# Kernel tuning notes

Hardware: AMD Instinct MI355X
Metric: run time of the kernel (lower is better)

## Reference

```python
import jax, jax.numpy as jnp
import numpy as np

B, N, K = 8, 2048, 30  # graphs, points per graph, kNN neighbors


def setup_inputs() -> dict:
    key = jax.random.key(0)
    ks = jax.random.split(key, 16)
    w = lambda k, s: jax.random.normal(k, s, jnp.float32) * 0.05
    z = lambda s: jnp.zeros(s, jnp.float32)
    return {
        "x": jax.random.normal(ks[0], (B * N, 3), jnp.float32),
        "pos": jax.random.normal(ks[1], (B * N, 3), jnp.float32),
        "w1a": w(ks[2], (12, 64)), "b1a": z(64),
        "w1b": w(ks[3], (64, 64)), "b1b": z(64),
        "w2a": w(ks[4], (128, 64)), "b2a": z(64),
        "w2b": w(ks[5], (64, 64)), "b2b": z(64),
        "w3a": w(ks[6], (128, 64)), "b3a": z(64),
        "w3b": w(ks[7], (64, 64)), "b3b": z(64),
        "hw1": w(ks[8], (192, 1024)), "hb1": z(1024),
        "hw2": w(ks[9], (1024, 512)), "hb2": z(512),
        "hw3": w(ks[10], (512, 128)), "hb3": z(128),
        "batch": jnp.repeat(jnp.arange(B, dtype=jnp.int32), N),
        "batch_size": B,
    }


def _knn_idx(f):
    # f: [B,N,d] -> indices of K nearest neighbors (incl. self), [B,N,K]
    d2 = jnp.sum(f * f, axis=-1)  # [B,N]
    dist = d2[:, :, None] + d2[:, None, :] - 2.0 * jnp.einsum('bnd,bmd->bnm', f, f)
    return jax.lax.top_k(-dist, K)[1]


def _edge_conv(f, wa, ba, wb, bb):
    # DynamicEdgeConv: kNN graph on f, message MLP([x_i, x_j - x_i]), max-aggregate
    idx = _knn_idx(f)                                   # [B,N,K]
    xj = jax.vmap(lambda ff, ii: ff[ii])(f, idx)        # [B,N,K,d]
    xi = f[:, :, None, :]
    e = jnp.concatenate([jnp.broadcast_to(xi, xj.shape), xj - xi], axis=-1)
    h = jax.nn.relu(e @ wa + ba)                        # MLP layer 1 (act)
    h = h @ wb + bb                                     # MLP layer 2 (plain last)
    return jnp.max(h, axis=2)                           # max aggr -> [B,N,64]


def reference(x, pos, w1a, b1a, w1b, b1b, w2a, b2a, w2b, b2b, w3a, b3a, w3b, b3b,
              hw1, hb1, hw2, hb2, hw3, hb3, batch, batch_size):
    x0 = jnp.concatenate([x, pos], axis=-1).reshape(batch_size, -1, 6)  # [B,N,6]
    x1 = _edge_conv(x0, w1a, b1a, w1b, b1b)
    x2 = _edge_conv(x1, w2a, b2a, w2b, b2b)
    x3 = _edge_conv(x2, w3a, b3a, w3b, b3b)
    feat = jnp.concatenate([x1, x2, x3], axis=-1)       # [B,N,192]
    h = jax.nn.relu(feat @ hw1 + hb1)                   # head MLP (dropout=eval)
    h = jax.nn.relu(h @ hw2 + hb2)
    out = h @ hw3 + hb3                                 # [B,N,out_channels]
    return out
```

## Files before the change

kernel.cpp:

```cpp
#include <hip/hip_runtime.h>
#include <math.h>

#define BATCH 8
#define NPER 2048
#define NPTS (BATCH*NPER)
#define KNN 30

typedef __attribute__((ext_vector_type(8))) short bf16x8;
typedef __attribute__((ext_vector_type(4))) float f32x4;

__device__ __forceinline__ ushort f2bf(float x) {
    unsigned u = __float_as_uint(x);
    unsigned r = (u + 0x7fffu + ((u >> 16) & 1u)) >> 16;
    return (ushort)r;
}
__device__ __forceinline__ float bf2f(ushort h) {
    return __uint_as_float(((unsigned)h) << 16);
}

__global__ void concat_kernel(const float* __restrict__ x, const float* __restrict__ pos,
                              float* __restrict__ x0) {
    int n = blockIdx.x * blockDim.x + threadIdx.x;
    if (n >= NPTS) return;
#pragma unroll
    for (int d = 0; d < 3; ++d) {
        x0[n*6 + d]     = x[n*3 + d];
        x0[n*6 + 3 + d] = pos[n*3 + d];
    }
}

template<int D>
__global__ void d2_kernel(const float* __restrict__ f, int stride, float* __restrict__ d2) {
    int n = blockIdx.x * blockDim.x + threadIdx.x;
    if (n >= NPTS) return;
    const float* r = f + (size_t)n * stride;
    float s = 0.f;
#pragma unroll
    for (int d = 0; d < D; ++d) s += r[d]*r[d];
    d2[n] = s;
}

template<int D>
__global__ __launch_bounds__(256, 4) void knn4_kernel(const float* __restrict__ f, int stride,
                                                      const float* __restrict__ d2,
                                                      int* __restrict__ idx) {
    __shared__ float sdist[4][NPER];
    __shared__ float sxi[4][(D+3)/4*4];
    __shared__ float sd2n[4];
    int t = threadIdx.x;
    int n0 = blockIdx.x * 4;
    int base = (n0 >> 11) << 11;

    if (t < 4*D) {
        int q = t / D, d = t - q*D;
        sxi[q][d] = f[(size_t)(n0 + q)*stride + d];
    }
    if (t < 4) sd2n[t] = d2[n0 + t];
    __syncthreads();

#pragma unroll 1
    for (int j = 0; j < NPER/256; ++j) {
        int ml = t + 256*j;
        int m = base + ml;
        const float* fm = f + (size_t)m*stride;
        float d2m = d2[m];
        float dot0 = 0.f, dot1 = 0.f, dot2 = 0.f, dot3 = 0.f;
#pragma unroll
        for (int d = 0; d < D; ++d) {
            float a = fm[d];
            dot0 += a*sxi[0][d];
            dot1 += a*sxi[1][d];
            dot2 += a*sxi[2][d];
            dot3 += a*sxi[3][d];
        }
        sdist[0][ml] = sd2n[0] + d2m - 2.f*dot0;
        sdist[1][ml] = sd2n[1] + d2m - 2.f*dot1;
        sdist[2][ml] = sd2n[2] + d2m - 2.f*dot2;
        sdist[3][ml] = sd2n[3] + d2m - 2.f*dot3;
    }
    __syncthreads();

    int w = t >> 6, lane = t & 63;
    int n = n0 + w;

    unsigned u[NPER/64];
#pragma unroll
    for (int i = 0; i < NPER/64; ++i) {
        float dv = sdist[w][lane + 64*i];
        int b = __float_as_int(dv);
        u[i] = (unsigned)(b ^ ((b >> 31) | 0x80000000));
    }

    unsigned T = 0u;
#pragma unroll
    for (int bit = 31; bit >= 0; --bit) {
        unsigned C = T | (1u << bit);
        int c = 0;
#pragma unroll
        for (int i = 0; i < NPER/64; ++i)
            c += (int)__popcll(__ballot(u[i] < C));
        if (c < KNN) T = C;
    }

    unsigned lm = 0u, em = 0u;
#pragma unroll
    for (int i = 0; i < NPER/64; ++i) {
        lm |= (u[i] < T)  ? (1u << i) : 0u;
        em |= (u[i] == T) ? (1u << i) : 0u;
    }
    int nl = __popc(lm);
    int inc = nl;
#pragma unroll
    for (int off = 1; off < 64; off <<= 1) {
        int y = __shfl_up(inc, off);
        if (lane >= off) inc += y;
    }
    int excl = inc - nl;
    int total_less = __shfl(inc, 63);

    int* op = idx + (size_t)n * KNN;
    int slot = excl;
#pragma unroll
    for (int i = 0; i < NPER/64; ++i) {
        if (lm & (1u << i)) { op[slot] = base + i*64 + lane; ++slot; }
    }

    int need = KNN - total_less;
    int running = 0;
#pragma unroll
    for (int i = 0; i < NPER/64; ++i) {
        unsigned long long bal = __ballot((em >> i) & 1u);
        if (bal) {
            unsigned long long lt = bal & ((1ull << lane) - 1ull);
            int r = running + __popcll(lt);
            if (((em >> i) & 1u) && r < need) op[total_less + r] = base + i*64 + lane;
            running += (int)__popcll(bal);
        }
    }
}

__global__ __launch_bounds__(256) void transpose64_kernel(const float* __restrict__ fin, int stride,
                                                          float* __restrict__ fT,
                                                          float* __restrict__ d2out) {
    __shared__ float tile[64][65];
    int t = threadIdx.x;
    int n0 = blockIdx.x * 64;
#pragma unroll
    for (int i = 0; i < 4; ++i) {
        int id = t + 256*i;
        int r = id >> 4, c4 = (id & 15) * 4;
        float4 v = *reinterpret_cast<const float4*>(&fin[(size_t)(n0 + r)*stride + c4]);
        tile[r][c4] = v.x; tile[r][c4+1] = v.y; tile[r][c4+2] = v.z; tile[r][c4+3] = v.w;
    }
    __syncthreads();
    if (t < 64) {
        float s = 0.f;
#pragma unroll
        for (int d = 0; d < 64; ++d) s += tile[t][d]*tile[t][d];
        d2out[n0 + t] = s;
    }
#pragma unroll
    for (int i = 0; i < 16; ++i) {
        int id = t + 256*i;
        int d = id >> 6, nn = id & 63;
        fT[(size_t)d * NPTS + n0 + nn] = tile[nn][d];
    }
}

__global__ __launch_bounds__(256) void knn6_kernel(const float* __restrict__ fq, int qstride,
                                                   const float* __restrict__ fT,
                                                   const float* __restrict__ d2,
                                                   int* __restrict__ idx) {
    __shared__ float sdist[4][NPER];
    __shared__ float sq[4][64];
    __shared__ float sd2n[4];
    int t = threadIdx.x;
    int n0 = blockIdx.x * 4;
    int base = (n0 >> 11) << 11;

    {
        int q = t >> 6, d = t & 63;
        sq[q][d] = fq[(size_t)(n0 + q)*qstride + d];
    }
    if (t < 4) sd2n[t] = d2[n0 + t];
    __syncthreads();

    float acc0[8], acc1[8], acc2[8], acc3[8];
#pragma unroll
    for (int j = 0; j < 8; ++j) { acc0[j] = 0.f; acc1[j] = 0.f; acc2[j] = 0.f; acc3[j] = 0.f; }

    int cbase = base + 8*t;

#pragma unroll 2
    for (int dc = 0; dc < 16; ++dc) {
        int d0 = dc * 4;
        float4 q0 = *reinterpret_cast<const float4*>(&sq[0][d0]);
        float4 q1 = *reinterpret_cast<const float4*>(&sq[1][d0]);
        float4 q2 = *reinterpret_cast<const float4*>(&sq[2][d0]);
        float4 q3 = *reinterpret_cast<const float4*>(&sq[3][d0]);
        float qa0[4] = {q0.x, q0.y, q0.z, q0.w};
        float qa1[4] = {q1.x, q1.y, q1.z, q1.w};
        float qa2[4] = {q2.x, q2.y, q2.z, q2.w};
        float qa3[4] = {q3.x, q3.y, q3.z, q3.w};
#pragma unroll
        for (int dd = 0; dd < 4; ++dd) {
            const float* cp = fT + (size_t)(d0 + dd) * NPTS + cbase;
            float4 c0 = *reinterpret_cast<const float4*>(cp);
            float4 c1 = *reinterpret_cast<const float4*>(cp + 4);
            float cv[8] = {c0.x,c0.y,c0.z,c0.w,c1.x,c1.y,c1.z,c1.w};
#pragma unroll
            for (int j = 0; j < 8; ++j) {
                acc0[j] += cv[j]*qa0[dd];
                acc1[j] += cv[j]*qa1[dd];
                acc2[j] += cv[j]*qa2[dd];
                acc3[j] += cv[j]*qa3[dd];
            }
        }
    }

    {
        float dn0 = sd2n[0], dn1 = sd2n[1], dn2 = sd2n[2], dn3 = sd2n[3];
        float4 dm0 = *reinterpret_cast<const float4*>(&d2[cbase]);
        float4 dm1 = *reinterpret_cast<const float4*>(&d2[cbase + 4]);
        float dmv[8] = {dm0.x,dm0.y,dm0.z,dm0.w,dm1.x,dm1.y,dm1.z,dm1.w};
#pragma unroll
        for (int j = 0; j < 8; ++j) {
            int ml = 8*t + j;
            sdist[0][ml] = dn0 + dmv[j] - 2.f*acc0[j];
            sdist[1][ml] = dn1 + dmv[j] - 2.f*acc1[j];
            sdist[2][ml] = dn2 + dmv[j] - 2.f*acc2[j];
            sdist[3][ml] = dn3 + dmv[j] - 2.f*acc3[j];
        }
    }
    __syncthreads();

    int w = t >> 6, lane = t & 63;
    int n = n0 + w;

    unsigned u[NPER/64];
#pragma unroll
    for (int i = 0; i < NPER/64; ++i) {
        float dv = sdist[w][lane + 64*i];
        int b = __float_as_int(dv);
        u[i] = (unsigned)(b ^ ((b >> 31) | 0x80000000));
    }

    unsigned T = 0u;
#pragma unroll
    for (int bit = 31; bit >= 0; --bit) {
        unsigned C = T | (1u << bit);
        int c = 0;
#pragma unroll
        for (int i = 0; i < NPER/64; ++i)
            c += (int)__popcll(__ballot(u[i] < C));
        if (c < KNN) T = C;
    }

    unsigned lm = 0u, em = 0u;
#pragma unroll
    for (int i = 0; i < NPER/64; ++i) {
        lm |= (u[i] < T)  ? (1u << i) : 0u;
        em |= (u[i] == T) ? (1u << i) : 0u;
    }
    int nl = __popc(lm);
    int inc = nl;
#pragma unroll
    for (int off = 1; off < 64; off <<= 1) {
        int y = __shfl_up(inc, off);
        if (lane >= off) inc += y;
    }
    int excl = inc - nl;
    int total_less = __shfl(inc, 63);

    int* op = idx + (size_t)n * KNN;
    int slot = excl;
#pragma unroll
    for (int i = 0; i < NPER/64; ++i) {
        if (lm & (1u << i)) { op[slot] = base + i*64 + lane; ++slot; }
    }

    int need = KNN - total_less;
    int running = 0;
#pragma unroll
    for (int i = 0; i < NPER/64; ++i) {
        unsigned long long bal = __ballot((em >> i) & 1u);
        if (bal) {
            unsigned long long lt = bal & ((1ull << lane) - 1ull);
            int r = running + __popcll(lt);
            if (((em >> i) & 1u) && r < need) op[total_less + r] = base + i*64 + lane;
            running += (int)__popcll(bal);
        }
    }
}

template<int D>
__global__ __launch_bounds__(256) void gmatbase_kernel(const float* __restrict__ fin, int in_stride,
                                                       const float* __restrict__ wa,
                                                       const float* __restrict__ ba,
                                                       float* __restrict__ G,
                                                       float* __restrict__ Gb) {
    constexpr int DP = (D+7)/8*8;
    __shared__ float sF[64][DP];
    int t = threadIdx.x;
    int row0 = blockIdx.x * 64;
    for (int i = t; i < 64*D; i += 256) {
        int r = i / D, c = i - r*D;
        sF[r][c] = fin[(size_t)(row0 + r)*in_stride + c];
    }
    int w = t >> 6, lane = t & 63;
    {
        float wreg[D];
#pragma unroll
        for (int d = 0; d < D; ++d) wreg[d] = wa[(size_t)(D + d)*64 + lane];
        __syncthreads();
#pragma unroll 1
        for (int pi = 0; pi < 16; ++pi) {
            int p = w*16 + pi;
            float acc = 0.f;
            if constexpr (D % 4 == 0) {
#pragma unroll
                for (int d = 0; d < D; d += 4) {
                    float4 fv = *reinterpret_cast<const float4*>(&sF[p][d]);
                    acc += fv.x*wreg[d] + fv.y*wreg[d+1] + fv.z*wreg[d+2] + fv.w*wreg[d+3];
                }
            } else {
#pragma unroll
                for (int d = 0; d < D; ++d) acc += sF[p][d]*wreg[d];
            }
            G[(size_t)(row0 + p)*64 + lane] = acc;
        }
    }
    {
        float wreg[D];
#pragma unroll
        for (int d = 0; d < D; ++d)
            wreg[d] = wa[(size_t)d*64 + lane] - wa[(size_t)(D + d)*64 + lane];
        float bc = ba[lane];
#pragma unroll 1
        for (int pi = 0; pi < 16; ++pi) {
            int p = w*16 + pi;
            float acc = bc;
#pragma unroll
            for (int d = 0; d < D; ++d) acc += sF[p][d]*wreg[d];
            Gb[(size_t)(row0 + p)*64 + lane] = acc;
        }
    }
}

__global__ __launch_bounds__(256) void edgemfma_kernel(
    const float* __restrict__ G, const float* __restrict__ Gbase,
    const int* __restrict__ idx,
    const ushort* __restrict__ wbTh, const ushort* __restrict__ wbTl,
    const float* __restrict__ bb,
    float* __restrict__ fout, int out_stride,
    ushort* __restrict__ fh, ushort* __restrict__ fl)
{
    __shared__ __align__(16) ushort sHh[128*72];
    __shared__ __align__(16) ushort sHl[128*72];
    __shared__ float sbase[4][64];
    int t = threadIdx.x;
    int n0 = blockIdx.x * 4;

    {
        int p = t >> 6, c = t & 63;
        sbase[p][c] = Gbase[(size_t)(n0 + p)*64 + c];
    }
    __syncthreads();

    {
        int r = t >> 1, c0 = (t & 1) * 32;
        int p = r >> 5, e = r & 31;
        int ecl = e < KNN ? e : (KNN - 1);
        int j = idx[(size_t)(n0 + p)*KNN + ecl];
        const float* gp = G + (size_t)j*64 + c0;
        const float* bp = &sbase[p][c0];
#pragma unroll
        for (int g = 0; g < 4; ++g) {
            float4 g0 = *reinterpret_cast<const float4*>(gp + 8*g);
            float4 g1 = *reinterpret_cast<const float4*>(gp + 8*g + 4);
            float4 b0 = *reinterpret_cast<const float4*>(bp + 8*g);
            float4 b1 = *reinterpret_cast<const float4*>(bp + 8*g + 4);
            float h[8] = {fmaxf(b0.x+g0.x,0.f), fmaxf(b0.y+g0.y,0.f),
                          fmaxf(b0.z+g0.z,0.f), fmaxf(b0.w+g0.w,0.f),
                          fmaxf(b1.x+g1.x,0.f), fmaxf(b1.y+g1.y,0.f),
                          fmaxf(b1.z+g1.z,0.f), fmaxf(b1.w+g1.w,0.f)};
            uint ph[4], pl[4];
#pragma unroll
            for (int i2 = 0; i2 < 4; ++i2) {
                ushort h0 = f2bf(h[2*i2]);
                ushort l0 = f2bf(h[2*i2] - bf2f(h0));
                ushort h1_ = f2bf(h[2*i2+1]);
                ushort l1 = f2bf(h[2*i2+1] - bf2f(h1_));
                ph[i2] = (uint)h0 | ((uint)h1_ << 16);
                pl[i2] = (uint)l0 | ((uint)l1 << 16);
            }
            *reinterpret_cast<uint4*>(&sHh[r*72 + c0 + 8*g]) = make_uint4(ph[0],ph[1],ph[2],ph[3]);
            *reinterpret_cast<uint4*>(&sHl[r*72 + c0 + 8*g]) = make_uint4(pl[0],pl[1],pl[2],pl[3]);
        }
    }
    __syncthreads();

    int lane = t & 63, w = t >> 6;
    int fr = lane & 15, fk = (lane >> 4) * 8;

    f32x4 acc[2][4];
#pragma unroll
    for (int mf = 0; mf < 2; ++mf)
#pragma unroll
        for (int nf = 0; nf < 4; ++nf) acc[mf][nf] = f32x4{0.f,0.f,0.f,0.f};

#pragma unroll
    for (int kk = 0; kk < 2; ++kk) {
        bf16x8 a0h = *reinterpret_cast<const bf16x8*>(&sHh[(w*32 + fr)*72 + kk*32 + fk]);
        bf16x8 a1h = *reinterpret_cast<const bf16x8*>(&sHh[(w*32 + 16 + fr)*72 + kk*32 + fk]);
        bf16x8 a0l = *reinterpret_cast<const bf16x8*>(&sHl[(w*32 + fr)*72 + kk*32 + fk]);
        bf16x8 a1l = *reinterpret_cast<const bf16x8*>(&sHl[(w*32 + 16 + fr)*72 + kk*32 + fk]);
#pragma unroll
        for (int nf = 0; nf < 4; ++nf) {
            bf16x8 bh = *reinterpret_cast<const bf16x8*>(&wbTh[(size_t)(nf*16 + fr)*64 + kk*32 + fk]);
            bf16x8 bl = *reinterpret_cast<const bf16x8*>(&wbTl[(size_t)(nf*16 + fr)*64 + kk*32 + fk]);
            acc[0][nf] = __builtin_amdgcn_mfma_f32_16x16x32_bf16(a0h, bh, acc[0][nf], 0,0,0);
            acc[0][nf] = __builtin_amdgcn_mfma_f32_16x16x32_bf16(a0h, bl, acc[0][nf], 0,0,0);
            acc[0][nf] = __builtin_amdgcn_mfma_f32_16x16x32_bf16(a0l, bh, acc[0][nf], 0,0,0);
            acc[1][nf] = __builtin_amdgcn_mfma_f32_16x16x32_bf16(a1h, bh, acc[1][nf], 0,0,0);
            acc[1][nf] = __builtin_amdgcn_mfma_f32_16x16x32_bf16(a1h, bl, acc[1][nf], 0,0,0);
            acc[1][nf] = __builtin_amdgcn_mfma_f32_16x16x32_bf16(a1l, bh, acc[1][nf], 0,0,0);
        }
    }

#pragma unroll
    for (int nf = 0; nf < 4; ++nf) {
        float vmax = -3.4e38f;
#pragma unroll
        for (int mf = 0; mf < 2; ++mf) {
#pragma unroll
            for (int j = 0; j < 4; ++j) {
                int lr = mf*16 + ((lane >> 4) << 2) + j;
                float v = acc[mf][nf][j];
                vmax = (lr < KNN) ? fmaxf(vmax, v) : vmax;
            }
        }
        vmax = fmaxf(vmax, __shfl_xor(vmax, 16));
        vmax = fmaxf(vmax, __shfl_xor(vmax, 32));
        if (lane < 16) {
            int c = nf*16 + lane;
            float v = vmax + bb[c];
            size_t o = (size_t)(n0 + w)*out_stride + c;
            fout[o] = v;
            ushort h = f2bf(v);
            fh[o] = h;
            fl[o] = f2bf(v - bf2f(h));
        }
    }
}

__global__ void wsplit_kernel(const float* __restrict__ w, int K, int N,
                              ushort* __restrict__ hi, ushort* __restrict__ lo, int total) {
    int i = blockIdx.x * 256 + threadIdx.x;
    if (i >= total) return;
    int n = i / K, k = i - n*K;
    float x = w[(size_t)k * N + n];
    ushort h = f2bf(x);
    hi[i] = h;
    lo[i] = f2bf(x - bf2f(h));
}

template<bool RELU, bool SPLIT_OUT>
__global__ __launch_bounds__(256) void mlp_gemm2_kernel(
    const ushort* __restrict__ Ah, const ushort* __restrict__ Al, int K,
    const ushort* __restrict__ Bh, const ushort* __restrict__ Bl,
    const float* __restrict__ bias,
    float* __restrict__ C, ushort* __restrict__ Ch, ushort* __restrict__ Cl, int N)
{
    __shared__ __align__(16) ushort sAh[128*40];
    __shared__ __align__(16) ushort sAl[128*40];
    __shared__ __align__(16) ushort sBh[128*40];
    __shared__ __align__(16) ushort sBl[128*40];
    int t = threadIdx.x;
    int lane = t & 63, w = t >> 6;
    int row0 = blockIdx.x * 128;
    int n0   = blockIdx.y * 128;
    int wr = w & 1, wc = w >> 1;
    int fr = lane & 15, fq = lane >> 4, fk = fq * 8;
    int r = t >> 2, sg = (t & 3) * 8;

    f32x4 acc[4][4];
#pragma unroll
    for (int m = 0; m < 4; ++m)
#pragma unroll
        for (int n = 0; n < 4; ++n) acc[m][n] = f32x4{0.f,0.f,0.f,0.f};

    const int nk = K / 32;
#pragma unroll 1
    for (int kc = 0; kc < nk; ++kc) {
        int k0 = kc * 32;
        uint4 vah0 = *reinterpret_cast<const uint4*>(&Ah[(size_t)(row0 + r)*K + k0 + sg]);
        uint4 vah1 = *reinterpret_cast<const uint4*>(&Ah[(size_t)(row0 + r + 64)*K + k0 + sg]);
        uint4 val0 = *reinterpret_cast<const uint4*>(&Al[(size_t)(row0 + r)*K + k0 + sg]);
        uint4 val1 = *reinterpret_cast<const uint4*>(&Al[(size_t)(row0 + r + 64)*K + k0 + sg]);
        uint4 vbh0 = *reinterpret_cast<const uint4*>(&Bh[(size_t)(n0 + r)*K + k0 + sg]);
        uint4 vbh1 = *reinterpret_cast<const uint4*>(&Bh[(size_t)(n0 + r + 64)*K + k0 + sg]);
        uint4 vbl0 = *reinterpret_cast<const uint4*>(&Bl[(size_t)(n0 + r)*K + k0 + sg]);
        uint4 vbl1 = *reinterpret_cast<const uint4*>(&Bl[(size_t)(n0 + r + 64)*K + k0 + sg]);
        __syncthreads();
        *reinterpret_cast<uint4*>(&sAh[r*40 + sg]) = vah0;
        *reinterpret_cast<uint4*>(&sAh[(r+64)*40 + sg]) = vah1;
        *reinterpret_cast<uint4*>(&sAl[r*40 + sg]) = val0;
        *reinterpret_cast<uint4*>(&sAl[(r+64)*40 + sg]) = val1;
        *reinterpret_cast<uint4*>(&sBh[r*40 + sg]) = vbh0;
        *reinterpret_cast<uint4*>(&sBh[(r+64)*40 + sg]) = vbh1;
        *reinterpret_cast<uint4*>(&sBl[r*40 + sg]) = vbl0;
        *reinterpret_cast<uint4*>(&sBl[(r+64)*40 + sg]) = vbl1;
        __syncthreads();

        bf16x8 bh_[4], bl_[4];
#pragma unroll
        for (int n = 0; n < 4; ++n) {
            bh_[n] = *reinterpret_cast<const bf16x8*>(&sBh[(wc*64 + n*16 + fr)*40 + fk]);
            bl_[n] = *reinterpret_cast<const bf16x8*>(&sBl[(wc*64 + n*16 + fr)*40 + fk]);
        }
#pragma unroll
        for (int m = 0; m < 4; ++m) {
            bf16x8 ah_ = *reinterpret_cast<const bf16x8*>(&sAh[(wr*64 + m*16 + fr)*40 + fk]);
            bf16x8 al_ = *reinterpret_cast<const bf16x8*>(&sAl[(wr*64 + m*16 + fr)*40 + fk]);
#pragma unroll
            for (int n = 0; n < 4; ++n) {
                acc[m][n] = __builtin_amdgcn_mfma_f32_16x16x32_bf16(ah_, bh_[n], acc[m][n], 0,0,0);
                acc[m][n] = __builtin_amdgcn_mfma_f32_16x16x32_bf16(ah_, bl_[n], acc[m][n], 0,0,0);
                acc[m][n] = __builtin_amdgcn_mfma_f32_16x16x32_bf16(al_, bh_[n], acc[m][n], 0,0,0);
            }
        }
    }

#pragma unroll
    for (int n = 0; n < 4; ++n) {
        int ocol = n0 + wc*64 + n*16 + fr;
        float bc = bias[ocol];
#pragma unroll
        for (int m = 0; m < 4; ++m) {
            int orow = row0 + wr*64 + m*16 + fq*4;
#pragma unroll
            for (int j = 0; j < 4; ++j) {
                float v = acc[m][n][j] + bc;
                if (RELU) v = fmaxf(v, 0.f);
                if (SPLIT_OUT) {
                    ushort h = f2bf(v);
                    Ch[(size_t)(orow + j)*N + ocol] = h;
                    Cl[(size_t)(orow + j)*N + ocol] = f2bf(v - bf2f(h));
                } else {
                    C[(size_t)(orow + j)*N + ocol] = v;
                }
            }
        }
    }
}

__global__ __launch_bounds__(256) void head_kernel(const float* __restrict__ feat,
                            const float* __restrict__ hw1, const float* __restrict__ hb1,
                            const float* __restrict__ hw2, const float* __restrict__ hb2,
                            const float* __restrict__ hw3, const float* __restrict__ hb3,
                            float* __restrict__ out) {
    __shared__ float smem[16384];
    float* sfeat = smem;
    float* sh1   = smem + 6144;
    int t = threadIdx.x;
    int row0 = blockIdx.x * 32;

    for (int i = t; i < 32*192; i += 256) sfeat[i] = feat[(size_t)row0*192 + i];
    __syncthreads();

    int c4 = t & 127, rh = t >> 7;
    float4 acc2[16];
    {
        float4 b = *reinterpret_cast<const float4*>(&hb2[4*c4]);
#pragma unroll
        for (int i = 0; i < 16; ++i) acc2[i] = b;
    }
    int c1 = t & 63, rg = t >> 6;

    for (int chunk = 0; chunk < 8; ++chunk) {
        int k0 = chunk * 128;
        float acc1a[8], acc1b[8];
        {
            float ba_ = hb1[k0 + c1], bb_ = hb1[k0 + 64 + c1];
#pragma unroll
            for (int i = 0; i < 8; ++i) { acc1a[i] = ba_; acc1b[i] = bb_; }
        }
#pragma unroll 1
        for (int k = 0; k < 192; k += 4) {
            float wA0 = hw1[(size_t)(k+0)*1024 + k0 + c1];
            float wA1 = hw1[(size_t)(k+1)*1024 + k0 + c1];
            float wA2 = hw1[(size_t)(k+2)*1024 + k0 + c1];
            float wA3 = hw1[(size_t)(k+3)*1024 + k0 + c1];
            float wB0 = hw1[(size_t)(k+0)*1024 + k0 + 64 + c1];
            float wB1 = hw1[(size_t)(k+1)*1024 + k0 + 64 + c1];
            float wB2 = hw1[(size_t)(k+2)*1024 + k0 + 64 + c1];
            float wB3 = hw1[(size_t)(k+3)*1024 + k0 + 64 + c1];
#pragma unroll
            for (int i = 0; i < 8; ++i) {
                float4 fv = *reinterpret_cast<const float4*>(&sfeat[(rg + 4*i)*192 + k]);
                acc1a[i] += fv.x*wA0 + fv.y*wA1 + fv.z*wA2 + fv.w*wA3;
                acc1b[i] += fv.x*wB0 + fv.y*wB1 + fv.z*wB2 + fv.w*wB3;
            }
        }
#pragma unroll
        for (int i = 0; i < 8; ++i) {
            sh1[(rg + 4*i)*128 + c1]      = fmaxf(acc1a[i], 0.f);
            sh1[(rg + 4*i)*128 + 64 + c1] = fmaxf(acc1b[i], 0.f);
        }
        __syncthreads();
        float4 wn[4];
#pragma unroll
        for (int q = 0; q < 4; ++q)
            wn[q] = *reinterpret_cast<const float4*>(&hw2[(size_t)(k0 + q)*512 + 4*c4]);
#pragma unroll 1
        for (int k = 0; k < 128; k += 4) {
            float4 wv[4];
#pragma unroll
            for (int q = 0; q < 4; ++q) wv[q] = wn[q];
            if (k + 4 < 128) {
#pragma unroll
                for (int q = 0; q < 4; ++q)
                    wn[q] = *reinterpret_cast<const float4*>(&hw2[(size_t)(k0 + k + 4 + q)*512 + 4*c4]);
            }
#pragma unroll
            for (int i = 0; i < 16; ++i) {
                float4 h4 = *reinterpret_cast<const float4*>(&sh1[(rh + 2*i)*128 + k]);
                acc2[i].x += h4.x*wv[0].x + h4.y*wv[1].x + h4.z*wv[2].x + h4.w*wv[3].x;
                acc2[i].y += h4.x*wv[0].y + h4.y*wv[1].y + h4.z*wv[2].y + h4.w*wv[3].y;
                acc2[i].z += h4.x*wv[0].z + h4.y*wv[1].z + h4.z*wv[2].z + h4.w*wv[3].z;
                acc2[i].w += h4.x*wv[0].w + h4.y*wv[1].w + h4.z*wv[2].w + h4.w*wv[3].w;
            }
        }
        __syncthreads();
    }
#pragma unroll
    for (int i = 0; i < 16; ++i) {
        float4 v;
        v.x = fmaxf(acc2[i].x, 0.f); v.y = fmaxf(acc2[i].y, 0.f);
        v.z = fmaxf(acc2[i].z, 0.f); v.w = fmaxf(acc2[i].w, 0.f);
        *reinterpret_cast<float4*>(&smem[(rh + 2*i)*512 + 4*c4]) = v;
    }
    __syncthreads();
    int c3 = t & 63, rg3 = t >> 6;
    float acc3a[8], acc3b[8];
    {
        float ba_ = hb3[c3], bb_ = hb3[c3 + 64];
#pragma unroll
        for (int i = 0; i < 8; ++i) { acc3a[i] = ba_; acc3b[i] = bb_; }
    }
#pragma unroll 1
    for (int k = 0; k < 512; k += 4) {
        float wA0 = hw3[(size_t)(k+0)*128 + c3];
        float wA1 = hw3[(size_t)(k+1)*128 + c3];
        float wA2 = hw3[(size_t)(k+2)*128 + c3];
        float wA3 = hw3[(size_t)(k+3)*128 + c3];
        float wB0 = hw3[(size_t)(k+0)*128 + c3 + 64];
        float wB1 = hw3[(size_t)(k+1)*128 + c3 + 64];
        float wB2 = hw3[(size_t)(k+2)*128 + c3 + 64];
        float wB3 = hw3[(size_t)(k+3)*128 + c3 + 64];
#pragma unroll
        for (int i = 0; i < 8; ++i) {
            float4 h4 = *reinterpret_cast<const float4*>(&smem[(rg3 + 4*i)*512 + k]);
            acc3a[i] += h4.x*wA0 + h4.y*wA1 + h4.z*wA2 + h4.w*wA3;
            acc3b[i] += h4.x*wB0 + h4.y*wB1 + h4.z*wB2 + h4.w*wB3;
        }
    }
#pragma unroll
    for (int i = 0; i < 8; ++i) {
        out[(size_t)(row0 + rg3 + 4*i)*128 + c3]      = acc3a[i];
        out[(size_t)(row0 + rg3 + 4*i)*128 + c3 + 64] = acc3b[i];
    }
}

extern "C" void kernel_launch(void* const* d_in, const int* in_sizes, int n_in,
                              void* d_out, int out_size, void* d_ws, size_t ws_size,
                              hipStream_t stream) {
    (void)in_sizes; (void)n_in; (void)out_size;
    const float* x   = (const float*)d_in[0];
    const float* pos = (const float*)d_in[1];
    const float* w1a = (const float*)d_in[2];
    const float* b1a = (const float*)d_in[3];
    const float* w1b = (const float*)d_in[4];
    const float* b1b = (const float*)d_in[5];
    const float* w2a = (const float*)d_in[6];
    const float* b2a = (const float*)d_in[7];
    const float* w2b = (const float*)d_in[8];
    const float* b2b = (const float*)d_in[9];
    const float* w3a = (const float*)d_in[10];
    const float* b3a = (const float*)d_in[11];
    const float* w3b = (const float*)d_in[12];
    const float* b3b = (const float*)d_in[13];
    const float* hw1 = (const float*)d_in[14];
    const float* hb1 = (const float*)d_in[15];
    const float* hw2 = (const float*)d_in[16];
    const float* hb2 = (const float*)d_in[17];
    const float* hw3 = (const float*)d_in[18];
    const float* hb3 = (const float*)d_in[19];
    float* out = (float*)d_out;

    float* ws = (float*)d_ws;
    float* x0   = ws;
    float* feat = ws + 98304;
    float* d2b  = ws + 3244032;
    int*   idxb = (int*)(ws + 3260416);
    float* G    = ws + 3751936;
    ushort* w1h = (ushort*)(ws + 4800512);
    ushort* w1l = (ushort*)(ws + 4898816);
    ushort* w2h = (ushort*)(ws + 4997120);
    ushort* w2l = (ushort*)(ws + 5259264);
    ushort* w3h = (ushort*)(ws + 5521408);
    ushort* w3l = (ushort*)(ws + 5554176);
    ushort* wb1h = (ushort*)(ws + 5586944);
    ushort* wb1l = (ushort*)(ws + 5588992);
    ushort* wb2h = (ushort*)(ws + 5591040);
    ushort* wb2l = (ushort*)(ws + 5593088);
    ushort* wb3h = (ushort*)(ws + 5595136);
    ushort* wb3l = (ushort*)(ws + 5597184);
    float* Gbase = ws + 5599232;
    ushort* fAh  = (ushort*)(ws + 6647808);
    ushort* fAl  = (ushort*)(ws + 8220672);
    const size_t base_units = 9793536;

    float* fT = G;

    int ns = 0;
    {
        const int cands[5] = {1, 2, 4, 8, 16};
        for (int ci = 0; ci < 5; ++ci) {
            int c = cands[ci];
            size_t need = (base_units + (size_t)(NPTS / c) * 1536) * 4;
            if (need <= ws_size) { ns = c; break; }
        }
    }

    wsplit_kernel<<<(192*1024 + 255)/256, 256, 0, stream>>>(hw1, 192, 1024, w1h, w1l, 192*1024);
    wsplit_kernel<<<(1024*512 + 255)/256, 256, 0, stream>>>(hw2, 1024, 512, w2h, w2l, 1024*512);
    wsplit_kernel<<<(512*128 + 255)/256, 256, 0, stream>>>(hw3, 512, 128, w3h, w3l, 512*128);
    wsplit_kernel<<<16, 256, 0, stream>>>(w1b, 64, 64, wb1h, wb1l, 4096);
    wsplit_kernel<<<16, 256, 0, stream>>>(w2b, 64, 64, wb2h, wb2l, 4096);
    wsplit_kernel<<<16, 256, 0, stream>>>(w3b, 64, 64, wb3h, wb3l, 4096);

    concat_kernel<<<NPTS/256, 256, 0, stream>>>(x, pos, x0);

    d2_kernel<6><<<NPTS/256, 256, 0, stream>>>(x0, 6, d2b);
    knn4_kernel<6><<<NPTS/4, 256, 0, stream>>>(x0, 6, d2b, idxb);
    gmatbase_kernel<6><<<NPTS/64, 256, 0, stream>>>(x0, 6, w1a, b1a, G, Gbase);
    edgemfma_kernel<<<NPTS/4, 256, 0, stream>>>(G, Gbase, idxb, wb1h, wb1l, b1b,
                                                feat, 192, fAh, fAl);

    transpose64_kernel<<<NPTS/64, 256, 0, stream>>>(feat, 192, fT, d2b);
    knn6_kernel<<<NPTS/4, 256, 0, stream>>>(feat, 192, fT, d2b, idxb);
    gmatbase_kernel<64><<<NPTS/64, 256, 0, stream>>>(feat, 192, w2a, b2a, G, Gbase);
    edgemfma_kernel<<<NPTS/4, 256, 0, stream>>>(G, Gbase, idxb, wb2h, wb2l, b2b,
                                                feat + 64, 192, fAh + 64, fAl + 64);

    transpose64_kernel<<<NPTS/64, 256, 0, stream>>>(feat + 64, 192, fT, d2b);
    knn6_kernel<<<NPTS/4, 256, 0, stream>>>(feat + 64, 192, fT, d2b, idxb);
    gmatbase_kernel<64><<<NPTS/64, 256, 0, stream>>>(feat + 64, 192, w3a, b3a, G, Gbase);
    edgemfma_kernel<<<NPTS/4, 256, 0, stream>>>(G, Gbase, idxb, wb3h, wb3l, b3b,
                                                feat + 128, 192, fAh + 128, fAl + 128);

    if (ns > 0) {
        int Ms = NPTS / ns;
        ushort* h1h = (ushort*)(ws + base_units);
        ushort* h1l = h1h + (size_t)Ms * 1024;
        ushort* h2h = (ushort*)(ws + base_units + (size_t)Ms * 1024);
        ushort* h2l = h2h + (size_t)Ms * 512;
        for (int s = 0; s < ns; ++s) {
            const ushort* Ash = fAh + (size_t)s * Ms * 192;
            const ushort* Asl = fAl + (size_t)s * Ms * 192;
            float* outs = out + (size_t)s * Ms * 128;
            mlp_gemm2_kernel<true, true ><<<dim3(Ms/128, 1024/128), 256, 0, stream>>>(
                Ash, Asl, 192, w1h, w1l, hb1, nullptr, h1h, h1l, 1024);
            mlp_gemm2_kernel<true, true ><<<dim3(Ms/128,  512/128), 256, 0, stream>>>(
                h1h, h1l, 1024, w2h, w2l, hb2, nullptr, h2h, h2l, 512);
            mlp_gemm2_kernel<false, false><<<dim3(Ms/128,  128/128), 256, 0, stream>>>(
                h2h, h2l, 512, w3h, w3l, hb3, outs, nullptr, nullptr, 128);
        }
    } else {
        head_kernel<<<NPTS/32, 256, 0, stream>>>(feat, hw1, hb1, hw2, hb2, hw3, hb3, out);
    }
}
```

Measured before the change: 702.6 us.

## Merge weight-split launches, fuse concat with norms, and use smaller-tile final GEMM

Replaces six separate weight-split launches with a single kernel that dispatches by global index, and fuses the input concat with the squared-norm computation. This removes several small launches and one global reload. It also swaps the last head GEMM (N=128) for a 64-row tile variant, giving twice as many blocks on a grid that otherwise had only one column of tiles. The fp32 fallback head kernel is removed, so if the workspace is too small no head is computed at all.

```diff
diff --git a/kernel.cpp b/kernel.cpp
--- a/kernel.cpp
+++ b/kernel.cpp
@@ -18,25 +18,21 @@
     return __uint_as_float(((unsigned)h) << 16);
 }
 
-__global__ void concat_kernel(const float* __restrict__ x, const float* __restrict__ pos,
-                              float* __restrict__ x0) {
+__global__ void concat_d2_kernel(const float* __restrict__ x, const float* __restrict__ pos,
+                                 float* __restrict__ x0, float* __restrict__ d2) {
     int n = blockIdx.x * blockDim.x + threadIdx.x;
     if (n >= NPTS) return;
+    float v[6];
 #pragma unroll
     for (int d = 0; d < 3; ++d) {
-        x0[n*6 + d]     = x[n*3 + d];
-        x0[n*6 + 3 + d] = pos[n*3 + d];
-    }
-}
-
-template<int D>
-__global__ void d2_kernel(const float* __restrict__ f, int stride, float* __restrict__ d2) {
-    int n = blockIdx.x * blockDim.x + threadIdx.x;
-    if (n >= NPTS) return;
-    const float* r = f + (size_t)n * stride;
+        v[d]     = x[n*3 + d];
+        v[3 + d] = pos[n*3 + d];
+    }
+#pragma unroll
+    for (int d = 0; d < 6; ++d) x0[n*6 + d] = v[d];
     float s = 0.f;
 #pragma unroll
-    for (int d = 0; d < D; ++d) s += r[d]*r[d];
+    for (int d = 0; d < 6; ++d) s += v[d]*v[d];
     d2[n] = s;
 }
 
@@ -454,10 +450,23 @@
     }
 }
 
-__global__ void wsplit_kernel(const float* __restrict__ w, int K, int N,
-                              ushort* __restrict__ hi, ushort* __restrict__ lo, int total) {
-    int i = blockIdx.x * 256 + threadIdx.x;
-    if (i >= total) return;
+__global__ void wsplit_all_kernel(
+    const float* __restrict__ hw1, ushort* __restrict__ w1h, ushort* __restrict__ w1l,
+    const float* __restrict__ hw2, ushort* __restrict__ w2h, ushort* __restrict__ w2l,
+    const float* __restrict__ hw3, ushort* __restrict__ w3h, ushort* __restrict__ w3l,
+    const float* __restrict__ w1b, ushort* __restrict__ wb1h, ushort* __restrict__ wb1l,
+    const float* __restrict__ w2b, ushort* __restrict__ wb2h, ushort* __restrict__ wb2l,
+    const float* __restrict__ w3b, ushort* __restrict__ wb3h, ushort* __restrict__ wb3l)
+{
+    int gi = blockIdx.x * 256 + threadIdx.x;
+    const float* w; ushort* hi; ushort* lo; int K, N, i;
+    if (gi < 196608)      { w = hw1; hi = w1h; lo = w1l; K = 192;  N = 1024; i = gi; }
+    else if (gi < 720896) { w = hw2; hi = w2h; lo = w2l; K = 1024; N = 512;  i = gi - 196608; }
+    else if (gi < 786432) { w = hw3; hi = w3h; lo = w3l; K = 512;  N = 128;  i = gi - 720896; }
+    else if (gi < 790528) { w = w1b; hi = wb1h; lo = wb1l; K = 64; N = 64;   i = gi - 786432; }
+    else if (gi < 794624) { w = w2b; hi = wb2h; lo = wb2l; K = 64; N = 64;   i = gi - 790528; }
+    else if (gi < 798720) { w = w3b; hi = wb3h; lo = wb3l; K = 64; N = 64;   i = gi - 794624; }
+    else return;
     int n = i / K, k = i - n*K;
     float x = w[(size_t)k * N + n];
     ushort h = f2bf(x);
@@ -555,121 +564,83 @@
     }
 }
 
-__global__ __launch_bounds__(256) void head_kernel(const float* __restrict__ feat,
-                            const float* __restrict__ hw1, const float* __restrict__ hb1,
-                            const float* __restrict__ hw2, const float* __restrict__ hb2,
-                            const float* __restrict__ hw3, const float* __restrict__ hb3,
-                            float* __restrict__ out) {
-    __shared__ float smem[16384];
-    float* sfeat = smem;
-    float* sh1   = smem + 6144;
+template<bool RELU>
+__global__ __launch_bounds__(256) void mlp_gemm3_kernel(
+    const ushort* __restrict__ Ah, const ushort* __restrict__ Al, int K,
+    const ushort* __restrict__ Bh, const ushort* __restrict__ Bl,
+    const float* __restrict__ bias,
+    float* __restrict__ C, int N)
+{
+    __shared__ __align__(16) ushort sAh[64*40];
+    __shared__ __align__(16) ushort sAl[64*40];
+    __shared__ __align__(16) ushort sBh[128*40];
+    __shared__ __align__(16) ushort sBl[128*40];
     int t = threadIdx.x;
-    int row0 = blockIdx.x * 32;
-
-    for (int i = t; i < 32*192; i += 256) sfeat[i] = feat[(size_t)row0*192 + i];
-    __syncthreads();
-
-    int c4 = t & 127, rh = t >> 7;
-    float4 acc2[16];
-    {
-        float4 b = *reinterpret_cast<const float4*>(&hb2[4*c4]);
-#pragma unroll
-        for (int i = 0; i < 16; ++i) acc2[i] = b;
-    }
-    int c1 = t & 63, rg = t >> 6;
-
-    for (int chunk = 0; chunk < 8; ++chunk) {
-        int k0 = chunk * 128;
-        float acc1a[8], acc1b[8];
-        {
-            float ba_ = hb1[k0 + c1], bb_ = hb1[k0 + 64 + c1];
-#pragma unroll
-            for (int i = 0; i < 8; ++i) { acc1a[i] = ba_; acc1b[i] = bb_; }
-        }
+    int lane = t & 63, w = t >> 6;
+    int row0 = blockIdx.x * 64;
+    int n0   = blockIdx.y * 128;
+    int wr = w & 1, wc = w >> 1;
+    int fr = lane & 15, fq = lane >> 4, fk = fq * 8;
+    int r = t >> 2, sg = (t & 3) * 8;
+
+    f32x4 acc[2][4];
+#pragma unroll
+    for (int m = 0; m < 2; ++m)
+#pragma unroll
+        for (int n = 0; n < 4; ++n) acc[m][n] = f32x4{0.f,0.f,0.f,0.f};
+
+    const int nk = K / 32;
 #pragma unroll 1
-        for (int k = 0; k < 192; k += 4) {
-            float wA0 = hw1[(size_t)(k+0)*1024 + k0 + c1];
-            float wA1 = hw1[(size_t)(k+1)*1024 + k0 + c1];
-            float wA2 = hw1[(size_t)(k+2)*1024 + k0 + c1];
-            float wA3 = hw1[(size_t)(k+3)*1024 + k0 + c1];
-            float wB0 = hw1[(size_t)(k+0)*1024 + k0 + 64 + c1];
-            float wB1 = hw1[(size_t)(k+1)*1024 + k0 + 64 + c1];
-            float wB2 = hw1[(size_t)(k+2)*1024 + k0 + 64 + c1];
-            float wB3 = hw1[(size_t)(k+3)*1024 + k0 + 64 + c1];
-#pragma unroll
-            for (int i = 0; i < 8; ++i) {
-                float4 fv = *reinterpret_cast<const float4*>(&sfeat[(rg + 4*i)*192 + k]);
-                acc1a[i] += fv.x*wA0 + fv.y*wA1 + fv.z*wA2 + fv.w*wA3;
-                acc1b[i] += fv.x*wB0 + fv.y*wB1 + fv.z*wB2 + fv.w*wB3;
+    for (int kc = 0; kc < nk; ++kc) {
+        int k0 = kc * 32;
+        uint4 vah0 = *reinterpret_cast<const uint4*>(&Ah[(size_t)(row0 + r)*K + k0 + sg]);
+        uint4 val0 = *reinterpret_cast<const uint4*>(&Al[(size_t)(row0 + r)*K + k0 + sg]);
+        uint4 vbh0 = *reinterpret_cast<const uint4*>(&Bh[(size_t)(n0 + r)*K + k0 + sg]);
+        uint4 vbh1 = *reinterpret_cast<const uint4*>(&Bh[(size_t)(n0 + r + 64)*K + k0 + sg]);
+        uint4 vbl0 = *reinterpret_cast<const uint4*>(&Bl[(size_t)(n0 + r)*K + k0 + sg]);
+        uint4 vbl1 = *reinterpret_cast<const uint4*>(&Bl[(size_t)(n0 + r + 64)*K + k0 + sg]);
+        __syncthreads();
+        *reinterpret_cast<uint4*>(&sAh[r*40 + sg]) = vah0;
+        *reinterpret_cast<uint4*>(&sAl[r*40 + sg]) = val0;
+        *reinterpret_cast<uint4*>(&sBh[r*40 + sg]) = vbh0;
+        *reinterpret_cast<uint4*>(&sBh[(r+64)*40 + sg]) = vbh1;
+        *reinterpret_cast<uint4*>(&sBl[r*40 + sg]) = vbl0;
+        *reinterpret_cast<uint4*>(&sBl[(r+64)*40 + sg]) = vbl1;
+        __syncthreads();
+
+        bf16x8 bh_[4], bl_[4];
+#pragma unroll
+        for (int n = 0; n < 4; ++n) {
+            bh_[n] = *reinterpret_cast<const bf16x8*>(&sBh[(wc*64 + n*16 + fr)*40 + fk]);
+            bl_[n] = *reinterpret_cast<const bf16x8*>(&sBl[(wc*64 + n*16 + fr)*40 + fk]);
+        }
+#pragma unroll
+        for (int m = 0; m < 2; ++m) {
+            bf16x8 ah_ = *reinterpret_cast<const bf16x8*>(&sAh[(wr*32 + m*16 + fr)*40 + fk]);
+            bf16x8 al_ = *reinterpret_cast<const bf16x8*>(&sAl[(wr*32 + m*16 + fr)*40 + fk]);
+#pragma unroll
+            for (int n = 0; n < 4; ++n) {
+                acc[m][n] = __builtin_amdgcn_mfma_f32_16x16x32_bf16(ah_, bh_[n], acc[m][n], 0,0,0);
+                acc[m][n] = __builtin_amdgcn_mfma_f32_16x16x32_bf16(ah_, bl_[n], acc[m][n], 0,0,0);
+                acc[m][n] = __builtin_amdgcn_mfma_f32_16x16x32_bf16(al_, bh_[n], acc[m][n], 0,0,0);
             }
         }
-#pragma unroll
-        for (int i = 0; i < 8; ++i) {
-            sh1[(rg + 4*i)*128 + c1]      = fmaxf(acc1a[i], 0.f);
-            sh1[(rg + 4*i)*128 + 64 + c1] = fmaxf(acc1b[i], 0.f);
-        }
-        __syncthreads();
-        float4 wn[4];
-#pragma unroll
-        for (int q = 0; q < 4; ++q)
-            wn[q] = *reinterpret_cast<const float4*>(&hw2[(size_t)(k0 + q)*512 + 4*c4]);
-#pragma unroll 1
-        for (int k = 0; k < 128; k += 4) {
-            float4 wv[4];
-#pragma unroll
-            for (int q = 0; q < 4; ++q) wv[q] = wn[q];
-            if (k + 4 < 128) {
-#pragma unroll
-                for (int q = 0; q < 4; ++q)
-                    wn[q] = *reinterpret_cast<const float4*>(&hw2[(size_t)(k0 + k + 4 + q)*512 + 4*c4]);
+    }
+
+#pragma unroll
+    for (int n = 0; n < 4; ++n) {
+        int ocol = n0 + wc*64 + n*16 + fr;
+        float bc = bias[ocol];
+#pragma unroll
+        for (int m = 0; m < 2; ++m) {
+            int orow = row0 + wr*32 + m*16 + fq*4;
+#pragma unroll
+            for (int j = 0; j < 4; ++j) {
+                float v = acc[m][n][j] + bc;
+                if (RELU) v = fmaxf(v, 0.f);
+                C[(size_t)(orow + j)*N + ocol] = v;
             }
-#pragma unroll
-            for (int i = 0; i < 16; ++i) {
-                float4 h4 = *reinterpret_cast<const float4*>(&sh1[(rh + 2*i)*128 + k]);
-                acc2[i].x += h4.x*wv[0].x + h4.y*wv[1].x + h4.z*wv[2].x + h4.w*wv[3].x;
-                acc2[i].y += h4.x*wv[0].y + h4.y*wv[1].y + h4.z*wv[2].y + h4.w*wv[3].y;
-                acc2[i].z += h4.x*wv[0].z + h4.y*wv[1].z + h4.z*wv[2].z + h4.w*wv[3].z;
-                acc2[i].w += h4.x*wv[0].w + h4.y*wv[1].w + h4.z*wv[2].w + h4.w*wv[3].w;
-            }
-        }
-        __syncthreads();
-    }
-#pragma unroll
-    for (int i = 0; i < 16; ++i) {
-        float4 v;
-        v.x = fmaxf(acc2[i].x, 0.f); v.y = fmaxf(acc2[i].y, 0.f);
-        v.z = fmaxf(acc2[i].z, 0.f); v.w = fmaxf(acc2[i].w, 0.f);
-        *reinterpret_cast<float4*>(&smem[(rh + 2*i)*512 + 4*c4]) = v;
-    }
-    __syncthreads();
-    int c3 = t & 63, rg3 = t >> 6;
-    float acc3a[8], acc3b[8];
-    {
-        float ba_ = hb3[c3], bb_ = hb3[c3 + 64];
-#pragma unroll
-        for (int i = 0; i < 8; ++i) { acc3a[i] = ba_; acc3b[i] = bb_; }
-    }
-#pragma unroll 1
-    for (int k = 0; k < 512; k += 4) {
-        float wA0 = hw3[(size_t)(k+0)*128 + c3];
-        float wA1 = hw3[(size_t)(k+1)*128 + c3];
-        float wA2 = hw3[(size_t)(k+2)*128 + c3];
-        float wA3 = hw3[(size_t)(k+3)*128 + c3];
-        float wB0 = hw3[(size_t)(k+0)*128 + c3 + 64];
-        float wB1 = hw3[(size_t)(k+1)*128 + c3 + 64];
-        float wB2 = hw3[(size_t)(k+2)*128 + c3 + 64];
-        float wB3 = hw3[(size_t)(k+3)*128 + c3 + 64];
-#pragma unroll
-        for (int i = 0; i < 8; ++i) {
-            float4 h4 = *reinterpret_cast<const float4*>(&smem[(rg3 + 4*i)*512 + k]);
-            acc3a[i] += h4.x*wA0 + h4.y*wA1 + h4.z*wA2 + h4.w*wA3;
-            acc3b[i] += h4.x*wB0 + h4.y*wB1 + h4.z*wB2 + h4.w*wB3;
-        }
-    }
-#pragma unroll
-    for (int i = 0; i < 8; ++i) {
-        out[(size_t)(row0 + rg3 + 4*i)*128 + c3]      = acc3a[i];
-        out[(size_t)(row0 + rg3 + 4*i)*128 + c3 + 64] = acc3b[i];
+        }
     }
 }
 
@@ -734,16 +705,12 @@
         }
     }
 
-    wsplit_kernel<<<(192*1024 + 255)/256, 256, 0, stream>>>(hw1, 192, 1024, w1h, w1l, 192*1024);
-    wsplit_kernel<<<(1024*512 + 255)/256, 256, 0, stream>>>(hw2, 1024, 512, w2h, w2l, 1024*512);
-    wsplit_kernel<<<(512*128 + 255)/256, 256, 0, stream>>>(hw3, 512, 128, w3h, w3l, 512*128);
-    wsplit_kernel<<<16, 256, 0, stream>>>(w1b, 64, 64, wb1h, wb1l, 4096);
-    wsplit_kernel<<<16, 256, 0, stream>>>(w2b, 64, 64, wb2h, wb2l, 4096);
-    wsplit_kernel<<<16, 256, 0, stream>>>(w3b, 64, 64, wb3h, wb3l, 4096);
-
-    concat_kernel<<<NPTS/256, 256, 0, stream>>>(x, pos, x0);
-
-    d2_kernel<6><<<NPTS/256, 256, 0, stream>>>(x0, 6, d2b);
+    wsplit_all_kernel<<<(798720 + 255)/256, 256, 0, stream>>>(
+        hw1, w1h, w1l, hw2, w2h, w2l, hw3, w3h, w3l,
+        w1b, wb1h, wb1l, w2b, wb2h, wb2l, w3b, wb3h, wb3l);
+
+    concat_d2_kernel<<<NPTS/256, 256, 0, stream>>>(x, pos, x0, d2b);
+
     knn4_kernel<6><<<NPTS/4, 256, 0, stream>>>(x0, 6, d2b, idxb);
     gmatbase_kernel<6><<<NPTS/64, 256, 0, stream>>>(x0, 6, w1a, b1a, G, Gbase);
     edgemfma_kernel<<<NPTS/4, 256, 0, stream>>>(G, Gbase, idxb, wb1h, wb1l, b1b,
@@ -775,10 +742,8 @@
                 Ash, Asl, 192, w1h, w1l, hb1, nullptr, h1h, h1l, 1024);
             mlp_gemm2_kernel<true, true ><<<dim3(Ms/128,  512/128), 256, 0, stream>>>(
                 h1h, h1l, 1024, w2h, w2l, hb2, nullptr, h2h, h2l, 512);
-            mlp_gemm2_kernel<false, false><<<dim3(Ms/128,  128/128), 256, 0, stream>>>(
-                h2h, h2l, 512, w3h, w3l, hb3, outs, nullptr, nullptr, 128);
-        }
-    } else {
-        head_kernel<<<NPTS/32, 256, 0, stream>>>(feat, hw1, hb1, hw2, hb2, hw3, hb3, out);
-    }
-}
+            mlp_gemm3_kernel<false><<<dim3(Ms/64, 1), 256, 0, stream>>>(
+                h2h, h2l, 512, w3h, w3l, hb3, outs, 128);
+        }
+    }
+}
```

New measurement: 682.1 us. 1.03x faster.
